# Kernel tuning notes

Hardware: AMD Instinct MI355X
Metric: run time of the kernel (lower is better)

The kernel has to match this reference:

```python
import jax, jax.numpy as jnp
import numpy as np

B, S, H, I, E, TOP_K = 2, 2048, 768, 3072, 7, 2


def setup_inputs() -> dict:
    key = jax.random.key(0)
    ks = jax.random.split(key, 5)
    x = jax.random.normal(ks[0], (B, S, H), dtype=jnp.float32)
    # parameter init ~ torch Linear default scale (1/sqrt(fan_in))
    wg = jax.random.normal(ks[1], (H, E), dtype=jnp.float32) / np.sqrt(H)
    bg = jnp.zeros((E,), dtype=jnp.float32)
    w1 = jax.random.normal(ks[2], (E, H, I), dtype=jnp.float32) / np.sqrt(H)
    b1 = jnp.zeros((E, I), dtype=jnp.float32)
    w2 = jax.random.normal(ks[3], (E, I, H), dtype=jnp.float32) / np.sqrt(I)
    b2 = jnp.zeros((E, H), dtype=jnp.float32)
    return {"x": x, "wg": wg, "bg": bg, "w1": w1, "b1": b1, "w2": w2, "b2": b2}


def _gate_weights(gate_logits):
    # top-k mask: -inf everywhere except top-k slots, then softmax.
    # Equivalent: softmax over top-k values, scattered back into [.., E].
    vals, idx = jax.lax.top_k(gate_logits, TOP_K)           # [B,S,K]
    wk = jax.nn.softmax(vals, axis=-1)                       # [B,S,K]
    onehot = jax.nn.one_hot(idx, E, dtype=gate_logits.dtype)  # [B,S,K,E]
    return jnp.einsum('bsk,bske->bse', wk, onehot)           # [B,S,E]


def reference(x, wg, bg, w1, b1, w2, b2):
    gate_logits = jnp.einsum('bsh,he->bse', x, wg) + bg      # [B,S,E]
    gate_w = _gate_weights(gate_logits)                       # [B,S,E]
    # dense all-expert FFN (the module evaluates EVERY expert on every token)
    h = jnp.einsum('bsh,ehi->bsei', x, w1) + b1              # [B,S,E,I]
    h = jax.nn.gelu(h, approximate=False)                    # torch.nn.GELU (exact erf)
    expert_out = jnp.einsum('bsei,eih->bseh', h, w2) + b2    # [B,S,E,H]
    out = jnp.einsum('bseh,bse->bsh', expert_out, gate_w)    # weighted combine
    # dropout is identity in eval mode
    return (out, gate_w)
```

## Files before the change

kernel.cpp:

```cpp
#include <hip/hip_runtime.h>
#include <hip/hip_bf16.h>
#include <cmath>

#define NT 4096
#define HD 768
#define ID 3072
#define NE 7
#define NP 8192
#define TM 256
#define TN 256
#define BK 32
#define KS 2
#define NT2 (HD / TN)
#define SLOTS 108
#define FFN1_MT 39

using short8 = __attribute__((ext_vector_type(8))) short;
using f32x4  = __attribute__((ext_vector_type(4))) float;
typedef __hip_bfloat16 bf16;

typedef const __attribute__((address_space(1))) void* gas_ptr;
typedef __attribute__((address_space(3))) void* las_ptr;
#define GLDS(g, l) __builtin_amdgcn_global_load_lds((gas_ptr)(g), (las_ptr)(l), 16, 0, 0)

#define BAR()   asm volatile("s_barrier" ::: "memory")
#define WAITL() asm volatile("s_waitcnt lgkmcnt(0)" ::: "memory")
#define WV8()   asm volatile("s_waitcnt vmcnt(8)" ::: "memory")
#define WV4()   asm volatile("s_waitcnt vmcnt(4)" ::: "memory")
#define WV0()   asm volatile("s_waitcnt vmcnt(0)" ::: "memory")
#define SCHEDB() __builtin_amdgcn_sched_barrier(0)

__device__ inline float b2f(unsigned short u) {
  unsigned v = (unsigned)u << 16; float f; __builtin_memcpy(&f, &v, 4); return f;
}

__global__ __launch_bounds__(64) void gate_kernel(
    const float* __restrict__ x, const float* __restrict__ wg, const float* __restrict__ bg,
    float* __restrict__ gate_out, bf16* __restrict__ xb,
    float* __restrict__ pair_w, int* __restrict__ tokexp)
{
  int t = blockIdx.x;
  int lane = threadIdx.x;
  const float* xr = x + (size_t)t * HD;
  float acc[NE];
#pragma unroll
  for (int e = 0; e < NE; e++) acc[e] = 0.f;
#pragma unroll
  for (int j = 0; j < HD / 64; j++) {
    int h = lane + j * 64;
    float xv = xr[h];
    xb[(size_t)t * HD + h] = __float2bfloat16(xv);
    const float* wr = wg + (size_t)h * NE;
#pragma unroll
    for (int e = 0; e < NE; e++) acc[e] += xv * wr[e];
  }
#pragma unroll
  for (int e = 0; e < NE; e++) {
    float v = acc[e];
    for (int s = 32; s > 0; s >>= 1) v += __shfl_down(v, s, 64);
    acc[e] = v;
  }
  if (lane == 0) {
    float lg[NE];
#pragma unroll
    for (int e = 0; e < NE; e++) lg[e] = acc[e] + bg[e];
    int i0 = 0;
    for (int e = 1; e < NE; e++) if (lg[e] > lg[i0]) i0 = e;
    int i1 = -1;
    for (int e = 0; e < NE; e++) {
      if (e == i0) continue;
      if (i1 < 0 || lg[e] > lg[i1]) i1 = e;
    }
    float v0 = lg[i0], v1 = lg[i1];
    float e1 = expf(v1 - v0);
    float inv = 1.f / (1.f + e1);
    float w0 = inv, w1v = e1 * inv;
    float* go = gate_out + (size_t)t * NE;
#pragma unroll
    for (int e = 0; e < NE; e++) go[e] = 0.f;
    go[i0] = w0; go[i1] = w1v;
    pair_w[2 * t + 0] = w0;
    pair_w[2 * t + 1] = w1v;
    tokexp[2 * t + 0] = i0;
    tokexp[2 * t + 1] = i1;
  }
}

__global__ __launch_bounds__(256) void route_kernel(
    const int* __restrict__ tokexp, int* __restrict__ elist, int* __restrict__ counts)
{
  __shared__ int wcnt[4];
  int e = blockIdx.x;
  int tid = threadIdx.x, wv = tid >> 6, ln = tid & 63;
  int base = 0;
  for (int chunk = 0; chunk < NP; chunk += 256) {
    int p = chunk + tid;
    bool m = (tokexp[p] == e);
    unsigned long long bal = __ballot(m);
    if (ln == 0) wcnt[wv] = __popcll(bal);
    __syncthreads();
    int pre = 0;
#pragma unroll
    for (int w = 0; w < 4; w++) pre += (w < wv) ? wcnt[w] : 0;
    int rank = pre + __popcll(bal & ((1ull << ln) - 1ull));
    if (m) elist[e * NP + base + rank] = p;
    base += wcnt[0] + wcnt[1] + wcnt[2] + wcnt[3];
    __syncthreads();
  }
  if (tid == 0) counts[e] = base;
}

__global__ __launch_bounds__(256) void transpose_cvt_kernel(
    const float* __restrict__ src, bf16* __restrict__ dst, int K, int N)
{
  __shared__ float tile[64][65];
  int e = blockIdx.z;
  int n0 = blockIdx.x * 64;
  int k0 = blockIdx.y * 64;
  const float* s = src + (size_t)e * K * N;
  bf16* d = dst + (size_t)e * K * N;
  int t = threadIdx.x;
  {
    int kk = t >> 4;
    int nc = (t & 15) << 2;
#pragma unroll
    for (int r = 0; r < 4; r++) {
      int k = kk + r * 16;
      float4 v = *(const float4*)(s + (size_t)(k0 + k) * N + n0 + nc);
      tile[k][nc + 0] = v.x; tile[k][nc + 1] = v.y;
      tile[k][nc + 2] = v.z; tile[k][nc + 3] = v.w;
    }
  }
  __syncthreads();
  {
    int c = t & 15;
    int nbase = t >> 4;
#pragma unroll
    for (int r = 0; r < 4; r++) {
      int n = nbase + r * 16;
      bf16 tmp[4];
#pragma unroll
      for (int i = 0; i < 4; i++) tmp[i] = __float2bfloat16(tile[4 * c + i][n]);
      ushort4 u; __builtin_memcpy(&u, tmp, 8);
      *(ushort4*)(d + (size_t)(n0 + n) * K + k0 + 4 * c) = u;
    }
  }
}


__global__ __launch_bounds__(512, 2) void ffn1_kernel(
    const bf16* __restrict__ xb, const bf16* __restrict__ w1t, const float* __restrict__ b1,
    const int* __restrict__ counts, const int* __restrict__ elist, bf16* __restrict__ hbuf)
{
  __shared__ bf16 As[4][TM][BK];
  __shared__ bf16 Bs[4][TN][BK];
  __shared__ int plist[TM];

  int tid = threadIdx.x;
  int e, base = 0, cnt = 0, acct = 0;
  bool found = false;
  for (e = 0; e < NE; e++) {
    cnt = counts[e];
    int tiles = (cnt + TM - 1) / TM;
    if ((int)blockIdx.y < acct + tiles) { base = ((int)blockIdx.y - acct) * TM; found = true; break; }
    acct += tiles;
  }
  if (!found) return;

  if (tid < TM) {
    int r = base + tid;
    plist[tid] = (r < cnt) ? elist[e * NP + r] : -1;
  }
  __syncthreads();

  const int n0 = blockIdx.x * TN;
  const bf16* Bsrc = w1t + (size_t)e * ID * HD;

  int c0 = tid, c1 = tid + 512;
  int r0 = c0 >> 2, p0 = c0 & 3, k0 = p0 ^ ((r0 >> 1) & 3);
  int r1 = c1 >> 2, p1 = c1 & 3, k1 = p1 ^ ((r1 >> 1) & 3);
  int pr0 = plist[r0], pr1 = plist[r1];
  const bf16* a0 = xb + (size_t)((pr0 >= 0 ? pr0 : 0) >> 1) * HD + k0 * 8;
  const bf16* a1 = xb + (size_t)((pr1 >= 0 ? pr1 : 0) >> 1) * HD + k1 * 8;
  const bf16* b0 = Bsrc + (size_t)(n0 + r0) * HD + k0 * 8;
  const bf16* b1v = Bsrc + (size_t)(n0 + r1) * HD + k1 * 8;

#define STAGE_A1(t) do { bf16* d_ = &As[(t) & 3][0][0]; \
    GLDS(a0 + (t) * BK, d_ + c0 * 8); GLDS(a1 + (t) * BK, d_ + c1 * 8); } while (0)
#define STAGE_B1(t) do { bf16* d_ = &Bs[(t) & 3][0][0]; \
    GLDS(b0 + (t) * BK, d_ + c0 * 8); GLDS(b1v + (t) * BK, d_ + c1 * 8); } while (0)

  int wave = tid >> 6, lane = tid & 63;
  int wm = (wave >> 2) * 128, wn = (wave & 3) * 64;
  int lr = lane & 15, quad = lane >> 4;
  int ph = quad ^ ((lr >> 1) & 3);

  f32x4 acc[8][4] = {};
  const int NIT = HD / BK;

#pragma unroll
  for (int pt = 0; pt < 3; ++pt) { STAGE_A1(pt); STAGE_B1(pt); }

  for (int t = 0; t < NIT; ++t) {
    int q = t & 3;
    short8 af[4], bfr[4];
    if (t + 2 < NIT) { WV8(); } else if (t + 1 < NIT) { WV4(); } else { WV0(); }
    BAR();
#pragma unroll
    for (int mm = 0; mm < 4; ++mm) af[mm] = *(const short8*)&As[q][wm + mm * 16 + lr][ph * 8];
#pragma unroll
    for (int nj = 0; nj < 4; ++nj) bfr[nj] = *(const short8*)&Bs[q][wn + nj * 16 + lr][ph * 8];
    if (t + 3 < NIT) STAGE_A1(t + 3);
    BAR();
    WAITL(); SCHEDB();
    __builtin_amdgcn_s_setprio(1);
#pragma unroll
    for (int mm = 0; mm < 4; ++mm)
#pragma unroll
      for (int nj = 0; nj < 4; ++nj)
        acc[mm][nj] = __builtin_amdgcn_mfma_f32_16x16x32_bf16(af[mm], bfr[nj], acc[mm][nj], 0, 0, 0);
    __builtin_amdgcn_s_setprio(0);
    BAR();
#pragma unroll
    for (int mm = 0; mm < 4; ++mm) af[mm] = *(const short8*)&As[q][wm + 64 + mm * 16 + lr][ph * 8];
    if (t + 3 < NIT) STAGE_B1(t + 3);
    BAR();
    WAITL(); SCHEDB();
    __builtin_amdgcn_s_setprio(1);
#pragma unroll
    for (int mm = 0; mm < 4; ++mm)
#pragma unroll
      for (int nj = 0; nj < 4; ++nj)
        acc[4 + mm][nj] = __builtin_amdgcn_mfma_f32_16x16x32_bf16(af[mm], bfr[nj], acc[4 + mm][nj], 0, 0, 0);
    __builtin_amdgcn_s_setprio(0);
  }
#undef STAGE_A1
#undef STAGE_B1

  const float* b1e = b1 + (size_t)e * ID;
#pragma unroll
  for (int nj = 0; nj < 4; ++nj) {
    int col = n0 + wn + nj * 16 + lr;
    float bias = b1e[col];
#pragma unroll
    for (int mi = 0; mi < 8; ++mi) {
#pragma unroll
      for (int r = 0; r < 4; ++r) {
        int mrow = wm + mi * 16 + quad * 4 + r;
        int p = plist[mrow];
        if (p >= 0) {
          float v = acc[mi][nj][r] + bias;
          float g = 0.5f * v * (1.0f + erff(v * 0.70710678118654752f));
          hbuf[(size_t)p * ID + col] = __float2bfloat16(g);
        }
      }
    }
  }
}

__global__ __launch_bounds__(512, 2) void ffn2_kernel(
    const bf16* __restrict__ hbuf, const bf16* __restrict__ w2t, const float* __restrict__ b2,
    const int* __restrict__ counts, const int* __restrict__ elist,
    const float* __restrict__ pair_w, bf16* __restrict__ pout)
{
  __shared__ bf16 As[4][TM][BK];
  __shared__ bf16 Bs[4][TN][BK];
  __shared__ int plist[TM];

  int tid = threadIdx.x;
  int xcd = blockIdx.x;
  int slot = blockIdx.y;
  int e = 0, seg = 0, base = 0, cnt = 0, n0 = 0;
  bool found = false;
  for (int p = xcd; p < 2 * NE; p += 8) {
    int pe = p >> 1;
    int c = counts[pe];
    int tiles = ((c + TM - 1) / TM) * NT2;
    if (slot < tiles) {
      e = pe; seg = p & 1; cnt = c;
      base = (slot / NT2) * TM;
      n0 = (slot % NT2) * TN;
      found = true; break;
    }
    slot -= tiles;
  }
  if (!found) return;

  if (tid < TM) {
    int r = base + tid;
    plist[tid] = (r < cnt) ? elist[e * NP + r] : -1;
  }
  __syncthreads();

  const int kbase = seg * (ID / KS);
  const bf16* Bsrc = w2t + (size_t)e * HD * ID;

  int c0 = tid, c1 = tid + 512;
  int r0 = c0 >> 2, p0 = c0 & 3, k0 = p0 ^ ((r0 >> 1) & 3);
  int r1 = c1 >> 2, p1 = c1 & 3, k1 = p1 ^ ((r1 >> 1) & 3);
  int pr0 = plist[r0], pr1 = plist[r1];
  const bf16* a0 = hbuf + (size_t)(pr0 >= 0 ? pr0 : 0) * ID + kbase + k0 * 8;
  const bf16* a1 = hbuf + (size_t)(pr1 >= 0 ? pr1 : 0) * ID + kbase + k1 * 8;
  const bf16* b0 = Bsrc + (size_t)(n0 + r0) * ID + kbase + k0 * 8;
  const bf16* b1v = Bsrc + (size_t)(n0 + r1) * ID + kbase + k1 * 8;

#define STAGE_A2(t) do { bf16* d_ = &As[(t) & 3][0][0]; \
    GLDS(a0 + (t) * BK, d_ + c0 * 8); GLDS(a1 + (t) * BK, d_ + c1 * 8); } while (0)
#define STAGE_B2(t) do { bf16* d_ = &Bs[(t) & 3][0][0]; \
    GLDS(b0 + (t) * BK, d_ + c0 * 8); GLDS(b1v + (t) * BK, d_ + c1 * 8); } while (0)

  int wave = tid >> 6, lane = tid & 63;
  int wm = (wave >> 2) * 128, wn = (wave & 3) * 64;
  int lr = lane & 15, quad = lane >> 4;
  int ph = quad ^ ((lr >> 1) & 3);

  f32x4 acc[8][4] = {};
  const int NIT = (ID / KS) / BK;

#pragma unroll
  for (int pt = 0; pt < 3; ++pt) { STAGE_A2(pt); STAGE_B2(pt); }

  for (int t = 0; t < NIT; ++t) {
    int q = t & 3;
    short8 af[4], bfr[4];
    if (t + 2 < NIT) { WV8(); } else if (t + 1 < NIT) { WV4(); } else { WV0(); }
    BAR();
#pragma unroll
    for (int mm = 0; mm < 4; ++mm) af[mm] = *(const short8*)&As[q][wm + mm * 16 + lr][ph * 8];
#pragma unroll
    for (int nj = 0; nj < 4; ++nj) bfr[nj] = *(const short8*)&Bs[q][wn + nj * 16 + lr][ph * 8];
    if (t + 3 < NIT) STAGE_A2(t + 3);
    BAR();
    WAITL(); SCHEDB();
    __builtin_amdgcn_s_setprio(1);
#pragma unroll
    for (int mm = 0; mm < 4; ++mm)
#pragma unroll
      for (int nj = 0; nj < 4; ++nj)
        acc[mm][nj] = __builtin_amdgcn_mfma_f32_16x16x32_bf16(af[mm], bfr[nj], acc[mm][nj], 0, 0, 0);
    __builtin_amdgcn_s_setprio(0);
    BAR();
#pragma unroll
    for (int mm = 0; mm < 4; ++mm) af[mm] = *(const short8*)&As[q][wm + 64 + mm * 16 + lr][ph * 8];
    if (t + 3 < NIT) STAGE_B2(t + 3);
    BAR();
    WAITL(); SCHEDB();
    __builtin_amdgcn_s_setprio(1);
#pragma unroll
    for (int mm = 0; mm < 4; ++mm)
#pragma unroll
      for (int nj = 0; nj < 4; ++nj)
        acc[4 + mm][nj] = __builtin_amdgcn_mfma_f32_16x16x32_bf16(af[mm], bfr[nj], acc[4 + mm][nj], 0, 0, 0);
    __builtin_amdgcn_s_setprio(0);
  }
#undef STAGE_A2
#undef STAGE_B2

  const float* b2e = b2 + (size_t)e * HD;
#pragma unroll
  for (int nj = 0; nj < 4; ++nj) {
    int col = n0 + wn + nj * 16 + lr;
    float bias = (seg == 0) ? b2e[col] : 0.f;
#pragma unroll
    for (int mi = 0; mi < 8; ++mi) {
#pragma unroll
      for (int r = 0; r < 4; ++r) {
        int mrow = wm + mi * 16 + quad * 4 + r;
        int p = plist[mrow];
        if (p >= 0) {
          float v = (acc[mi][nj][r] + bias) * pair_w[p];
          pout[((size_t)seg * NP + p) * HD + col] = __float2bfloat16(v);
        }
      }
    }
  }
}

__global__ __launch_bounds__(192) void combine_kernel(
    const bf16* __restrict__ pout, float* __restrict__ out)
{
  int t = blockIdx.x, j = threadIdx.x;
  f32x4 o = {0.f, 0.f, 0.f, 0.f};
#pragma unroll
  for (int s = 0; s < KS; s++) {
#pragma unroll
    for (int k = 0; k < 2; k++) {
      const ushort4* v = (const ushort4*)(pout + ((size_t)s * NP + 2 * t + k) * HD);
      ushort4 u = v[j];
      o[0] += b2f(u.x); o[1] += b2f(u.y); o[2] += b2f(u.z); o[3] += b2f(u.w);
    }
  }
  ((f32x4*)(out + (size_t)t * HD))[j] = o;
}

extern "C" void kernel_launch(void* const* d_in, const int* in_sizes, int n_in,
                              void* d_out, int out_size, void* d_ws, size_t ws_size,
                              hipStream_t stream)
{
  const float* x  = (const float*)d_in[0];
  const float* wg = (const float*)d_in[1];
  const float* bg = (const float*)d_in[2];
  const float* w1 = (const float*)d_in[3];
  const float* b1 = (const float*)d_in[4];
  const float* w2 = (const float*)d_in[5];
  const float* b2 = (const float*)d_in[6];
  float* out = (float*)d_out;
  float* gate_out = out + (size_t)NT * HD;

  char* ws = (char*)d_ws;
  size_t off = 0;
  int* counts  = (int*)(ws + off);  off += 256;
  int* tokexp  = (int*)(ws + off);  off += (size_t)NP * 4;
  int* elist   = (int*)(ws + off);  off += (size_t)NE * NP * 4;
  float* pair_w = (float*)(ws + off); off += (size_t)NP * 4;
  bf16* xb   = (bf16*)(ws + off);   off += (size_t)NT * HD * 2;
  bf16* w1t  = (bf16*)(ws + off);   off += (size_t)NE * HD * ID * 2;
  bf16* w2t  = (bf16*)(ws + off);   off += (size_t)NE * HD * ID * 2;
  bf16* hbuf = (bf16*)(ws + off);   off += (size_t)NP * ID * 2;
  bf16* pout = (bf16*)(ws + off);   off += (size_t)KS * NP * HD * 2;

  gate_kernel<<<NT, 64, 0, stream>>>(x, wg, bg, gate_out, xb, pair_w, tokexp);
  route_kernel<<<NE, 256, 0, stream>>>(tokexp, elist, counts);
  transpose_cvt_kernel<<<dim3(ID / 64, HD / 64, NE), 256, 0, stream>>>(w1, w1t, HD, ID);
  transpose_cvt_kernel<<<dim3(HD / 64, ID / 64, NE), 256, 0, stream>>>(w2, w2t, ID, HD);
  ffn1_kernel<<<dim3(ID / TN, FFN1_MT), 512, 0, stream>>>(xb, w1t, b1, counts, elist, hbuf);
  ffn2_kernel<<<dim3(8, SLOTS), 512, 0, stream>>>(hbuf, w2t, b2, counts, elist, pair_w, pout);
  combine_kernel<<<NT, 192, 0, stream>>>(pout, out);
}
```

Baseline: 393.0 us.

## Swap MFMA operands for row-wise vector epilogue, remap FFN1 grid per XCD, fast GELU

Swaps the MFMA A/B operands so each lane holds four consecutive columns of one row, letting the FFN1 and FFN2 epilogues write ushort4 vectors and read biases as float4 instead of scattered scalar stores. Remaps the FFN1 grid to one dimension with an XCD-aware block ordering so neighbouring tiles share an L2. Replaces erff with a polynomial erf approximation that uses a fast reciprocal and exp, and moves the vmcnt wait and barrier to the end of each iteration. Also lowers the FFN2 slot count; the polynomial GELU adds some approximation error.

```diff
diff --git a/kernel.cpp b/kernel.cpp
--- a/kernel.cpp
+++ b/kernel.cpp
@@ -12,8 +12,11 @@
 #define BK 32
 #define KS 2
 #define NT2 (HD / TN)
-#define SLOTS 108
+#define SLOTS 102
+#define NRING 4
 #define FFN1_MT 39
+#define FFN1_NT (ID / TN)
+#define FFN1_GRID (FFN1_NT * FFN1_MT)
 
 using short8 = __attribute__((ext_vector_type(8))) short;
 using f32x4  = __attribute__((ext_vector_type(4))) float;
@@ -32,6 +35,16 @@
 
 __device__ inline float b2f(unsigned short u) {
   unsigned v = (unsigned)u << 16; float f; __builtin_memcpy(&f, &v, 4); return f;
+}
+
+__device__ inline float gelu_erf(float v) {
+  float xa = fabsf(v) * 0.70710678118654752f;
+  float t  = __builtin_amdgcn_rcpf(1.0f + 0.3275911f * xa);
+  float p  = t * (0.254829592f + t * (-0.284496736f + t * (1.421413741f +
+             t * (-1.453152027f + t * 1.061405429f))));
+  float er = 1.0f - p * __expf(-xa * xa);
+  er = (v < 0.0f) ? -er : er;
+  return 0.5f * v * (1.0f + er);
 }
 
 __global__ __launch_bounds__(64) void gate_kernel(
@@ -152,17 +165,22 @@
     const bf16* __restrict__ xb, const bf16* __restrict__ w1t, const float* __restrict__ b1,
     const int* __restrict__ counts, const int* __restrict__ elist, bf16* __restrict__ hbuf)
 {
-  __shared__ bf16 As[4][TM][BK];
-  __shared__ bf16 Bs[4][TN][BK];
+  __shared__ bf16 As[NRING][TM][4][8];
+  __shared__ bf16 Bs[NRING][TN][4][8];
   __shared__ int plist[TM];
 
   int tid = threadIdx.x;
+  int raw = blockIdx.x;
+  int xcd = raw & 7, pos = raw >> 3;
+  int v = (xcd < 4) ? xcd * 59 + pos : 236 + (xcd - 4) * 58 + pos;
+  int by = v / FFN1_NT, bx = v % FFN1_NT;
+
   int e, base = 0, cnt = 0, acct = 0;
   bool found = false;
   for (e = 0; e < NE; e++) {
     cnt = counts[e];
     int tiles = (cnt + TM - 1) / TM;
-    if ((int)blockIdx.y < acct + tiles) { base = ((int)blockIdx.y - acct) * TM; found = true; break; }
+    if (by < acct + tiles) { base = (by - acct) * TM; found = true; break; }
     acct += tiles;
   }
   if (!found) return;
@@ -173,22 +191,24 @@
   }
   __syncthreads();
 
-  const int n0 = blockIdx.x * TN;
+  const int n0 = bx * TN;
   const bf16* Bsrc = w1t + (size_t)e * ID * HD;
 
   int c0 = tid, c1 = tid + 512;
-  int r0 = c0 >> 2, p0 = c0 & 3, k0 = p0 ^ ((r0 >> 1) & 3);
-  int r1 = c1 >> 2, p1 = c1 & 3, k1 = p1 ^ ((r1 >> 1) & 3);
+  int r0 = c0 >> 2, k0 = (c0 & 3) ^ ((r0 >> 1) & 3);
+  int r1 = c1 >> 2, k1 = (c1 & 3) ^ ((r1 >> 1) & 3);
   int pr0 = plist[r0], pr1 = plist[r1];
   const bf16* a0 = xb + (size_t)((pr0 >= 0 ? pr0 : 0) >> 1) * HD + k0 * 8;
   const bf16* a1 = xb + (size_t)((pr1 >= 0 ? pr1 : 0) >> 1) * HD + k1 * 8;
   const bf16* b0 = Bsrc + (size_t)(n0 + r0) * HD + k0 * 8;
   const bf16* b1v = Bsrc + (size_t)(n0 + r1) * HD + k1 * 8;
 
-#define STAGE_A1(t) do { bf16* d_ = &As[(t) & 3][0][0]; \
-    GLDS(a0 + (t) * BK, d_ + c0 * 8); GLDS(a1 + (t) * BK, d_ + c1 * 8); } while (0)
-#define STAGE_B1(t) do { bf16* d_ = &Bs[(t) & 3][0][0]; \
-    GLDS(b0 + (t) * BK, d_ + c0 * 8); GLDS(b1v + (t) * BK, d_ + c1 * 8); } while (0)
+#define STAGE_A(t_) do { bf16* d_ = (bf16*)As + (size_t)((t_) & 3) * TM * 32;    \
+    GLDS(a0 + (size_t)(t_) * BK, d_ + c0 * 8);                                   \
+    GLDS(a1 + (size_t)(t_) * BK, d_ + c1 * 8); } while (0)
+#define STAGE_B(t_) do { bf16* d_ = (bf16*)Bs + (size_t)((t_) & 3) * TN * 32;    \
+    GLDS(b0 + (size_t)(t_) * BK, d_ + c0 * 8);                                   \
+    GLDS(b1v + (size_t)(t_) * BK, d_ + c1 * 8); } while (0)
 
   int wave = tid >> 6, lane = tid & 63;
   int wm = (wave >> 2) * 128, wn = (wave & 3) * 64;
@@ -198,61 +218,65 @@
   f32x4 acc[8][4] = {};
   const int NIT = HD / BK;
 
-#pragma unroll
-  for (int pt = 0; pt < 3; ++pt) { STAGE_A1(pt); STAGE_B1(pt); }
+  STAGE_A(0); STAGE_B(0);
+  STAGE_A(1); STAGE_B(1);
+  STAGE_A(2); STAGE_B(2);
+  WV8(); BAR();
 
   for (int t = 0; t < NIT; ++t) {
     int q = t & 3;
     short8 af[4], bfr[4];
-    if (t + 2 < NIT) { WV8(); } else if (t + 1 < NIT) { WV4(); } else { WV0(); }
-    BAR();
-#pragma unroll
-    for (int mm = 0; mm < 4; ++mm) af[mm] = *(const short8*)&As[q][wm + mm * 16 + lr][ph * 8];
-#pragma unroll
-    for (int nj = 0; nj < 4; ++nj) bfr[nj] = *(const short8*)&Bs[q][wn + nj * 16 + lr][ph * 8];
-    if (t + 3 < NIT) STAGE_A1(t + 3);
+#pragma unroll
+    for (int mi = 0; mi < 4; mi++) af[mi] = *(const short8*)&As[q][wm + mi * 16 + lr][ph][0];
+#pragma unroll
+    for (int nj = 0; nj < 4; nj++) bfr[nj] = *(const short8*)&Bs[q][wn + nj * 16 + lr][ph][0];
+    if (t + 3 < NIT) STAGE_A(t + 3);
     BAR();
     WAITL(); SCHEDB();
     __builtin_amdgcn_s_setprio(1);
 #pragma unroll
-    for (int mm = 0; mm < 4; ++mm)
-#pragma unroll
-      for (int nj = 0; nj < 4; ++nj)
-        acc[mm][nj] = __builtin_amdgcn_mfma_f32_16x16x32_bf16(af[mm], bfr[nj], acc[mm][nj], 0, 0, 0);
+    for (int mi = 0; mi < 4; mi++)
+#pragma unroll
+      for (int nj = 0; nj < 4; nj++)
+        acc[mi][nj] = __builtin_amdgcn_mfma_f32_16x16x32_bf16(bfr[nj], af[mi], acc[mi][nj], 0, 0, 0);
     __builtin_amdgcn_s_setprio(0);
     BAR();
 #pragma unroll
-    for (int mm = 0; mm < 4; ++mm) af[mm] = *(const short8*)&As[q][wm + 64 + mm * 16 + lr][ph * 8];
-    if (t + 3 < NIT) STAGE_B1(t + 3);
+    for (int mi = 0; mi < 4; mi++) af[mi] = *(const short8*)&As[q][wm + 64 + mi * 16 + lr][ph][0];
+    if (t + 3 < NIT) STAGE_B(t + 3);
+    if (t + 3 < NIT) { WV8(); } else if (t + 2 < NIT) { WV4(); } else if (t + 1 < NIT) { WV0(); }
     BAR();
     WAITL(); SCHEDB();
     __builtin_amdgcn_s_setprio(1);
 #pragma unroll
-    for (int mm = 0; mm < 4; ++mm)
-#pragma unroll
-      for (int nj = 0; nj < 4; ++nj)
-        acc[4 + mm][nj] = __builtin_amdgcn_mfma_f32_16x16x32_bf16(af[mm], bfr[nj], acc[4 + mm][nj], 0, 0, 0);
+    for (int mi = 0; mi < 4; mi++)
+#pragma unroll
+      for (int nj = 0; nj < 4; nj++)
+        acc[4 + mi][nj] = __builtin_amdgcn_mfma_f32_16x16x32_bf16(bfr[nj], af[mi], acc[4 + mi][nj], 0, 0, 0);
     __builtin_amdgcn_s_setprio(0);
-  }
-#undef STAGE_A1
-#undef STAGE_B1
+    BAR();
+  }
+#undef STAGE_A
+#undef STAGE_B
 
   const float* b1e = b1 + (size_t)e * ID;
 #pragma unroll
-  for (int nj = 0; nj < 4; ++nj) {
-    int col = n0 + wn + nj * 16 + lr;
-    float bias = b1e[col];
-#pragma unroll
-    for (int mi = 0; mi < 8; ++mi) {
-#pragma unroll
-      for (int r = 0; r < 4; ++r) {
-        int mrow = wm + mi * 16 + quad * 4 + r;
-        int p = plist[mrow];
-        if (p >= 0) {
-          float v = acc[mi][nj][r] + bias;
-          float g = 0.5f * v * (1.0f + erff(v * 0.70710678118654752f));
-          hbuf[(size_t)p * ID + col] = __float2bfloat16(g);
-        }
+  for (int mi = 0; mi < 8; mi++) {
+    int mrow = wm + mi * 16 + lr;
+    int p = plist[mrow];
+    if (p >= 0) {
+      bf16* drow = hbuf + (size_t)p * ID;
+#pragma unroll
+      for (int nj = 0; nj < 4; nj++) {
+        int colb = n0 + wn + nj * 16 + (quad << 2);
+        float4 bs = *(const float4*)(b1e + colb);
+        bf16 o[4];
+        o[0] = __float2bfloat16(gelu_erf(acc[mi][nj][0] + bs.x));
+        o[1] = __float2bfloat16(gelu_erf(acc[mi][nj][1] + bs.y));
+        o[2] = __float2bfloat16(gelu_erf(acc[mi][nj][2] + bs.z));
+        o[3] = __float2bfloat16(gelu_erf(acc[mi][nj][3] + bs.w));
+        ushort4 u; __builtin_memcpy(&u, o, 8);
+        *(ushort4*)(drow + colb) = u;
       }
     }
   }
@@ -263,8 +287,8 @@
     const int* __restrict__ counts, const int* __restrict__ elist,
     const float* __restrict__ pair_w, bf16* __restrict__ pout)
 {
-  __shared__ bf16 As[4][TM][BK];
-  __shared__ bf16 Bs[4][TN][BK];
+  __shared__ bf16 As[NRING][TM][4][8];
+  __shared__ bf16 Bs[NRING][TN][4][8];
   __shared__ int plist[TM];
 
   int tid = threadIdx.x;
@@ -296,18 +320,20 @@
   const bf16* Bsrc = w2t + (size_t)e * HD * ID;
 
   int c0 = tid, c1 = tid + 512;
-  int r0 = c0 >> 2, p0 = c0 & 3, k0 = p0 ^ ((r0 >> 1) & 3);
-  int r1 = c1 >> 2, p1 = c1 & 3, k1 = p1 ^ ((r1 >> 1) & 3);
+  int r0 = c0 >> 2, k0 = (c0 & 3) ^ ((r0 >> 1) & 3);
+  int r1 = c1 >> 2, k1 = (c1 & 3) ^ ((r1 >> 1) & 3);
   int pr0 = plist[r0], pr1 = plist[r1];
   const bf16* a0 = hbuf + (size_t)(pr0 >= 0 ? pr0 : 0) * ID + kbase + k0 * 8;
   const bf16* a1 = hbuf + (size_t)(pr1 >= 0 ? pr1 : 0) * ID + kbase + k1 * 8;
   const bf16* b0 = Bsrc + (size_t)(n0 + r0) * ID + kbase + k0 * 8;
   const bf16* b1v = Bsrc + (size_t)(n0 + r1) * ID + kbase + k1 * 8;
 
-#define STAGE_A2(t) do { bf16* d_ = &As[(t) & 3][0][0]; \
-    GLDS(a0 + (t) * BK, d_ + c0 * 8); GLDS(a1 + (t) * BK, d_ + c1 * 8); } while (0)
-#define STAGE_B2(t) do { bf16* d_ = &Bs[(t) & 3][0][0]; \
-    GLDS(b0 + (t) * BK, d_ + c0 * 8); GLDS(b1v + (t) * BK, d_ + c1 * 8); } while (0)
+#define STAGE_A(t_) do { bf16* d_ = (bf16*)As + (size_t)((t_) & 3) * TM * 32;    \
+    GLDS(a0 + (size_t)(t_) * BK, d_ + c0 * 8);                                   \
+    GLDS(a1 + (size_t)(t_) * BK, d_ + c1 * 8); } while (0)
+#define STAGE_B(t_) do { bf16* d_ = (bf16*)Bs + (size_t)((t_) & 3) * TN * 32;    \
+    GLDS(b0 + (size_t)(t_) * BK, d_ + c0 * 8);                                   \
+    GLDS(b1v + (size_t)(t_) * BK, d_ + c1 * 8); } while (0)
 
   int wave = tid >> 6, lane = tid & 63;
   int wm = (wave >> 2) * 128, wn = (wave & 3) * 64;
@@ -317,60 +343,70 @@
   f32x4 acc[8][4] = {};
   const int NIT = (ID / KS) / BK;
 
-#pragma unroll
-  for (int pt = 0; pt < 3; ++pt) { STAGE_A2(pt); STAGE_B2(pt); }
+  STAGE_A(0); STAGE_B(0);
+  STAGE_A(1); STAGE_B(1);
+  STAGE_A(2); STAGE_B(2);
+  WV8(); BAR();
 
   for (int t = 0; t < NIT; ++t) {
     int q = t & 3;
     short8 af[4], bfr[4];
-    if (t + 2 < NIT) { WV8(); } else if (t + 1 < NIT) { WV4(); } else { WV0(); }
-    BAR();
-#pragma unroll
-    for (int mm = 0; mm < 4; ++mm) af[mm] = *(const short8*)&As[q][wm + mm * 16 + lr][ph * 8];
-#pragma unroll
-    for (int nj = 0; nj < 4; ++nj) bfr[nj] = *(const short8*)&Bs[q][wn + nj * 16 + lr][ph * 8];
-    if (t + 3 < NIT) STAGE_A2(t + 3);
+#pragma unroll
+    for (int mi = 0; mi < 4; mi++) af[mi] = *(const short8*)&As[q][wm + mi * 16 + lr][ph][0];
+#pragma unroll
+    for (int nj = 0; nj < 4; nj++) bfr[nj] = *(const short8*)&Bs[q][wn + nj * 16 + lr][ph][0];
+    if (t + 3 < NIT) STAGE_A(t + 3);
     BAR();
     WAITL(); SCHEDB();
     __builtin_amdgcn_s_setprio(1);
 #pragma unroll
-    for (int mm = 0; mm < 4; ++mm)
-#pragma unroll
-      for (int nj = 0; nj < 4; ++nj)
-        acc[mm][nj] = __builtin_amdgcn_mfma_f32_16x16x32_bf16(af[mm], bfr[nj], acc[mm][nj], 0, 0, 0);
+    for (int mi = 0; mi < 4; mi++)
+#pragma unroll
+      for (int nj = 0; nj < 4; nj++)
+        acc[mi][nj] = __builtin_amdgcn_mfma_f32_16x16x32_bf16(bfr[nj], af[mi], acc[mi][nj], 0, 0, 0);
     __builtin_amdgcn_s_setprio(0);
     BAR();
 #pragma unroll
-    for (int mm = 0; mm < 4; ++mm) af[mm] = *(const short8*)&As[q][wm + 64 + mm * 16 + lr][ph * 8];
-    if (t + 3 < NIT) STAGE_B2(t + 3);
+    for (int mi = 0; mi < 4; mi++) af[mi] = *(const short8*)&As[q][wm + 64 + mi * 16 + lr][ph][0];
+    if (t + 3 < NIT) STAGE_B(t + 3);
+    if (t + 3 < NIT) { WV8(); } else if (t + 2 < NIT) { WV4(); } else if (t + 1 < NIT) { WV0(); }
     BAR();
     WAITL(); SCHEDB();
     __builtin_amdgcn_s_setprio(1);
 #pragma unroll
-    for (int mm = 0; mm < 4; ++mm)
-#pragma unroll
-      for (int nj = 0; nj < 4; ++nj)
-        acc[4 + mm][nj] = __builtin_amdgcn_mfma_f32_16x16x32_bf16(af[mm], bfr[nj], acc[4 + mm][nj], 0, 0, 0);
+    for (int mi = 0; mi < 4; mi++)
+#pragma unroll
+      for (int nj = 0; nj < 4; nj++)
+        acc[4 + mi][nj] = __builtin_amdgcn_mfma_f32_16x16x32_bf16(bfr[nj], af[mi], acc[4 + mi][nj], 0, 0, 0);
     __builtin_amdgcn_s_setprio(0);
-  }
-#undef STAGE_A2
-#undef STAGE_B2
+    BAR();
+  }
+#undef STAGE_A
+#undef STAGE_B
 
   const float* b2e = b2 + (size_t)e * HD;
 #pragma unroll
-  for (int nj = 0; nj < 4; ++nj) {
-    int col = n0 + wn + nj * 16 + lr;
-    float bias = (seg == 0) ? b2e[col] : 0.f;
-#pragma unroll
-    for (int mi = 0; mi < 8; ++mi) {
-#pragma unroll
-      for (int r = 0; r < 4; ++r) {
-        int mrow = wm + mi * 16 + quad * 4 + r;
-        int p = plist[mrow];
-        if (p >= 0) {
-          float v = (acc[mi][nj][r] + bias) * pair_w[p];
-          pout[((size_t)seg * NP + p) * HD + col] = __float2bfloat16(v);
+  for (int mi = 0; mi < 8; mi++) {
+    int mrow = wm + mi * 16 + lr;
+    int p = plist[mrow];
+    if (p >= 0) {
+      float pw = pair_w[p];
+      bf16* drow = pout + ((size_t)seg * NP + p) * HD;
+#pragma unroll
+      for (int nj = 0; nj < 4; nj++) {
+        int colb = n0 + wn + nj * 16 + (quad << 2);
+        float bx_ = 0.f, by_ = 0.f, bz_ = 0.f, bw_ = 0.f;
+        if (seg == 0) {
+          float4 bs = *(const float4*)(b2e + colb);
+          bx_ = bs.x; by_ = bs.y; bz_ = bs.z; bw_ = bs.w;
         }
+        bf16 o[4];
+        o[0] = __float2bfloat16((acc[mi][nj][0] + bx_) * pw);
+        o[1] = __float2bfloat16((acc[mi][nj][1] + by_) * pw);
+        o[2] = __float2bfloat16((acc[mi][nj][2] + bz_) * pw);
+        o[3] = __float2bfloat16((acc[mi][nj][3] + bw_) * pw);
+        ushort4 u; __builtin_memcpy(&u, o, 8);
+        *(ushort4*)(drow + colb) = u;
       }
     }
   }
@@ -423,7 +459,7 @@
   route_kernel<<<NE, 256, 0, stream>>>(tokexp, elist, counts);
   transpose_cvt_kernel<<<dim3(ID / 64, HD / 64, NE), 256, 0, stream>>>(w1, w1t, HD, ID);
   transpose_cvt_kernel<<<dim3(HD / 64, ID / 64, NE), 256, 0, stream>>>(w2, w2t, ID, HD);
-  ffn1_kernel<<<dim3(ID / TN, FFN1_MT), 512, 0, stream>>>(xb, w1t, b1, counts, elist, hbuf);
+  ffn1_kernel<<<FFN1_GRID, 512, 0, stream>>>(xb, w1t, b1, counts, elist, hbuf);
   ffn2_kernel<<<dim3(8, SLOTS), 512, 0, stream>>>(hbuf, w2t, b2, counts, elist, pair_w, pout);
   combine_kernel<<<NT, 192, 0, stream>>>(pout, out);
 }
```

Result: faster. 330.8 us (-15.8%).
